# Performance work log

Hardware: AMD Instinct MI355X
Metric: run time of the kernel (lower is better)

Reference implementation:

```python
import jax, jax.numpy as jnp
import numpy as np

NC = 151  # number of object classes (VG)
NR = 51   # number of relation classes (VG)


def setup_inputs() -> dict:
    key = jax.random.key(0)
    ks = jax.random.split(key, 10)
    B, N, D = 32, 100, 4096
    H = D // 4
    w = lambda k, shape, fan_in: (jax.random.normal(k, shape, jnp.float32) / np.sqrt(fan_in).astype(np.float32))
    return {
        "encoder_reps": jax.random.normal(ks[0], (B * N, D), jnp.float32),
        "W_comp": w(ks[1], (D, H), D),        # obj_comp Linear (no bias)
        "W_ou1": w(ks[2], (H, H), H),         # ou1 Linear
        "W_ofc": w(ks[3], (H, H), H),         # ofc_u Linear
        "W_decomp": w(ks[4], (H, D), H),      # obj_decomp Linear
        "conv1": w(ks[5], (10, NR, 3, 3), NR * 9),  # Conv2d(51,10,3,pad=1)
        "conv2": w(ks[6], (5, 10, 3, 3), 10 * 9),   # Conv2d(10,5,3,pad=1)
        "conv3": w(ks[7], (1, 5, 1, 1), 5),         # Conv2d(5,1,1)
        "freq_emb": jax.random.normal(ks[8], (NC * NC, NR), jnp.float32) * 0.01,
        "obj_preds": jax.random.randint(ks[9], (B * N,), 0, NC),
        "num_obj": 100,
    }


def reference(encoder_reps, W_comp, W_ou1, W_ofc, W_decomp, conv1, conv2, conv3, freq_emb, obj_preds, num_obj):
    T, D = encoder_reps.shape
    N = num_obj
    B = T // N
    relu = jax.nn.relu
    # obj_comp then per-image ou1 (vectorized over images)
    comp = relu(encoder_reps @ W_comp).reshape(B, N, -1)   # [B,N,H]
    obj_u1 = relu(comp @ W_ou1)                             # [B,N,H]
    # product-index frequency-bias gather: emb[subj*NC + obj]
    labels = obj_preds.reshape(B, N)
    pair_idx = labels[:, :, None] * NC + labels[:, None, :]  # [B,N,N]
    adj_fg = freq_emb[pair_idx]                               # [B,N,N,NR]
    # adjacency net: Conv-Conv-Conv-Tanh over the NxN 'image' with NR channels
    x = jnp.transpose(adj_fg, (0, 3, 1, 2))                   # [B,NR,N,N]
    dn = ("NCHW", "OIHW", "NCHW")
    x = jax.lax.conv_general_dilated(x, conv1, (1, 1), "SAME", dimension_numbers=dn)
    x = jax.lax.conv_general_dilated(x, conv2, (1, 1), "SAME", dimension_numbers=dn)
    x = jnp.tanh(jax.lax.conv_general_dilated(x, conv3, (1, 1), "SAME", dimension_numbers=dn))
    adj = x[:, 0]                                             # [B,N,N]
    # graph message passing: adj @ obj_u1, then ofc_u / decomp + residual
    ofl_u = jnp.einsum("bnm,bmh->bnh", adj, obj_u1).reshape(T, -1)
    u_m = relu(ofl_u @ W_ofc)
    decomp = relu(u_m @ W_decomp)
    return decomp + encoder_reps
```

## Files before the change

### kernel.cpp

```cpp
#include <hip/hip_runtime.h>
#include <cmath>

#define NCC 151
#define NRCH 51
#define BDIM 32
#define NOBJ 100
#define DDIM 4096
#define HDIM 1024
#define TDIM (BDIM * NOBJ)

typedef __bf16 bf16_t;
typedef __bf16 bf16x8 __attribute__((ext_vector_type(8)));
typedef __bf16 bf16x4 __attribute__((ext_vector_type(4)));
typedef float f32x4 __attribute__((ext_vector_type(4)));

template <bool RELU, bool ADDBF16, int SPLITK, int MODE>
__global__ __launch_bounds__(256) void gemm_bf16(
    const bf16_t* __restrict__ A,
    const bf16_t* __restrict__ Bt,
    const bf16_t* __restrict__ add,
    void* __restrict__ Cout,
    int N, int K, size_t MN) {
  __shared__ __align__(16) bf16_t Asm[2][128 * 64];
  __shared__ __align__(16) bf16_t Bsm[2][128 * 64];
  const int tid = threadIdx.x;
  const int lane = tid & 63;
  const int w = tid >> 6;
  const int wm = w >> 1, wn = w & 1;

  const int nx = gridDim.x, ny = gridDim.y, nz = gridDim.z;
  const int h = blockIdx.x + nx * (blockIdx.y + ny * blockIdx.z);
  int bx, by, bz;
  if (MODE == 3) {
    const int xcd = h & 7, s = h >> 3;
    bz = xcd >> 1;
    const int half = xcd & 1;
    if (half == 1 && s >= 96) return;
    const int c = s / 40;
    if (c < 2) {
      const int within = s % 40;
      bx = within / 5;
      by = (half ? 13 : 0) + c * 5 + within % 5;
    } else if (half == 0) {
      const int w2 = s - 80;
      bx = w2 / 3;
      by = 10 + w2 % 3;
    } else {
      const int w2 = s - 80;
      bx = w2 / 2;
      by = 23 + w2 % 2;
    }
  } else {
    const int nwg = nx * ny * nz;
    const int q = nwg >> 3;
    const int lin = (h & 7) * q + (h >> 3);
    by = lin % ny;
    const int r = lin / ny;
    bx = r % nx;
    bz = r / nx;
  }

  const int bm = by * 128, bn = bx * 128;
  const int lr = lane & 15;
  const int lk = lane >> 4;

  int kBeg = 0, kEnd = K;
  if (SPLITK > 1) {
    const int chunk = (((K / 64) + SPLITK - 1) / SPLITK) * 64;
    kBeg = bz * chunk;
    kEnd = min(K, kBeg + chunk);
  }

  f32x4 acc[4][4];
#pragma unroll
  for (int m = 0; m < 4; ++m)
#pragma unroll
    for (int n = 0; n < 4; ++n) acc[m][n] = (f32x4){0.f, 0.f, 0.f, 0.f};

  const int srow = tid >> 3;
  const int sslot = tid & 7;

  auto stage = [&](int buf, int kt) {
#pragma unroll
    for (int i = 0; i < 4; ++i) {
      const int row = i * 32 + srow;
      const int kc = sslot ^ (row & 7);
      const bf16_t* ga = A + (size_t)(bm + row) * K + kt + kc * 8;
      const bf16_t* gb = Bt + (size_t)(bn + row) * K + kt + kc * 8;
      __builtin_amdgcn_global_load_lds(
          (const __attribute__((address_space(1))) void*)ga,
          (__attribute__((address_space(3))) void*)((char*)&Asm[buf][0] +
                                                    i * 4096 + w * 1024),
          16, 0, 0);
      __builtin_amdgcn_global_load_lds(
          (const __attribute__((address_space(1))) void*)gb,
          (__attribute__((address_space(3))) void*)((char*)&Bsm[buf][0] +
                                                    i * 4096 + w * 1024),
          16, 0, 0);
    }
  };

  stage(0, kBeg);
  __syncthreads();

  int cur = 0;
  for (int kt = kBeg; kt < kEnd; kt += 64) {
    const bool more = (kt + 64 < kEnd);
    if (more) stage(cur ^ 1, kt + 64);

    char* ldsA = (char*)&Asm[cur][0];
    char* ldsB = (char*)&Bsm[cur][0];
    bf16x8 af[4][2], bfr[4][2];
#pragma unroll
    for (int m = 0; m < 4; ++m) {
      const int row = wm * 64 + m * 16 + lr;
#pragma unroll
      for (int kk = 0; kk < 2; ++kk) {
        const int slot = kk * 4 + lk;
        af[m][kk] =
            *(const bf16x8*)(ldsA + row * 128 + ((slot ^ (lr & 7)) << 4));
      }
    }
#pragma unroll
    for (int n = 0; n < 4; ++n) {
      const int row = wn * 64 + n * 16 + lr;
#pragma unroll
      for (int kk = 0; kk < 2; ++kk) {
        const int slot = kk * 4 + lk;
        bfr[n][kk] =
            *(const bf16x8*)(ldsB + row * 128 + ((slot ^ (lr & 7)) << 4));
      }
    }
#pragma unroll
    for (int m = 0; m < 4; ++m)
#pragma unroll
      for (int n = 0; n < 4; ++n) {
        acc[m][n] = __builtin_amdgcn_mfma_f32_16x16x32_bf16(
            af[m][0], bfr[n][0], acc[m][n], 0, 0, 0);
        acc[m][n] = __builtin_amdgcn_mfma_f32_16x16x32_bf16(
            af[m][1], bfr[n][1], acc[m][n], 0, 0, 0);
      }

    if (more) __syncthreads();
    cur ^= 1;
  }

  const int or0 = bm + wm * 64 + lk * 4;
  const int oc0 = bn + wn * 64 + lr;
#pragma unroll
  for (int m = 0; m < 4; ++m)
#pragma unroll
    for (int n = 0; n < 4; ++n)
#pragma unroll
      for (int r = 0; r < 4; ++r) {
        float v = acc[m][n][r];
        const size_t off = (size_t)(or0 + m * 16 + r) * N + (oc0 + n * 16);
        if (SPLITK > 1) {
          ((bf16_t*)Cout)[bz * MN + off] = (bf16_t)v;
        } else {
          if (RELU) v = fmaxf(v, 0.f);
          if (ADDBF16)
            ((float*)Cout)[off] = v + (float)add[off];
          else
            ((bf16_t*)Cout)[off] = (bf16_t)v;
        }
      }
}

template <int NPART>
__global__ __launch_bounds__(256) void reduceN_kernel(
    const bf16_t* __restrict__ p, bf16_t* __restrict__ out, int n8,
    size_t MN) {
  int i = blockIdx.x * 256 + threadIdx.x;
  if (i >= n8) return;
  float s[8] = {};
#pragma unroll
  for (int z = 0; z < NPART; ++z) {
    bf16x8 v = *(const bf16x8*)(p + z * MN + (size_t)i * 8);
#pragma unroll
    for (int j = 0; j < 8; ++j) s[j] += (float)v[j];
  }
  bf16x8 o;
#pragma unroll
  for (int j = 0; j < 8; ++j) o[j] = (bf16_t)fmaxf(s[j], 0.f);
  *(bf16x8*)(out + (size_t)i * 8) = o;
}

__global__ __launch_bounds__(256) void cvt_bf16_kernel(
    const float* __restrict__ in, bf16_t* __restrict__ out, int n4) {
  int i = blockIdx.x * 256 + threadIdx.x;
  if (i >= n4) return;
  float4 v = ((const float4*)in)[i];
  bf16x4 o = {(bf16_t)v.x, (bf16_t)v.y, (bf16_t)v.z, (bf16_t)v.w};
  ((bf16x4*)out)[i] = o;
}

__global__ __launch_bounds__(256) void transT_kernel(
    const float* __restrict__ in, bf16_t* __restrict__ out, int K, int N) {
  __shared__ float t[32][33];
  const int n0 = blockIdx.x * 32, k0 = blockIdx.y * 32;
  const int tx = threadIdx.x & 31, ty = threadIdx.x >> 5;
#pragma unroll
  for (int i = 0; i < 4; ++i)
    t[ty + i * 8][tx] = in[(size_t)(k0 + ty + i * 8) * N + n0 + tx];
  __syncthreads();
#pragma unroll
  for (int i = 0; i < 4; ++i)
    out[(size_t)(n0 + ty + i * 8) * K + k0 + tx] = (bf16_t)t[tx][ty + i * 8];
}

__global__ __launch_bounds__(256) void prep_w1r_kernel(
    const float* __restrict__ w1, float* __restrict__ w1r) {
  int idx = blockIdx.x * 256 + threadIdx.x;
  if (idx >= NRCH * 90) return;
  int ci = idx / 90, r = idx % 90, k9 = r / 10, co = r % 10;
  w1r[idx] = w1[((co * NRCH + ci) * 3 + k9 / 3) * 3 + (k9 % 3)];
}

__global__ __launch_bounds__(128) void femb1_kernel(
    const float* __restrict__ femb, const float* __restrict__ w1r,
    float* __restrict__ femb1) {
  __shared__ float row[NRCH];
  const int p = blockIdx.x;
  if (threadIdx.x < NRCH)
    row[threadIdx.x] = femb[(size_t)p * NRCH + threadIdx.x];
  __syncthreads();
  const int t = threadIdx.x;
  if (t >= 90) return;
  float acc = 0.f;
#pragma unroll
  for (int ci = 0; ci < NRCH; ++ci) acc += row[ci] * w1r[ci * 90 + t];
  femb1[((size_t)p * 9 + t / 10) * 12 + (t % 10)] = acc;
}

__global__ __launch_bounds__(256) void conv1g_kernel(
    const int* __restrict__ preds, const float* __restrict__ femb1,
    float* __restrict__ x1) {
  int idx = blockIdx.x * 256 + threadIdx.x;
  if (idx >= BDIM * NOBJ * NOBJ) return;
  int j = idx % NOBJ;
  int i = (idx / NOBJ) % NOBJ;
  int b = idx / (NOBJ * NOBJ);
  const int* pr = preds + b * NOBJ;
  int li[3], lj[3];
#pragma unroll
  for (int d = 0; d < 3; ++d) {
    li[d] = pr[min(max(i + d - 1, 0), NOBJ - 1)];
    lj[d] = pr[min(max(j + d - 1, 0), NOBJ - 1)];
  }
  f32x4 a0 = {0.f, 0.f, 0.f, 0.f}, a1 = a0, a2 = a0;
#pragma unroll
  for (int kh = 0; kh < 3; ++kh) {
    int ii = i + kh - 1;
    if (ii < 0 || ii >= NOBJ) continue;
#pragma unroll
    for (int kw = 0; kw < 3; ++kw) {
      int jj = j + kw - 1;
      if (jj < 0 || jj >= NOBJ) continue;
      int p = li[kh] * NCC + lj[kw];
      const f32x4* f =
          (const f32x4*)(femb1 + ((size_t)p * 9 + kh * 3 + kw) * 12);
      a0 += f[0];
      a1 += f[1];
      a2 += f[2];
    }
  }
  f32x4* o = (f32x4*)(x1 + (size_t)idx * 12);
  o[0] = a0;
  o[1] = a1;
  o[2] = a2;
}

__global__ __launch_bounds__(256) void conv23_kernel(
    const float* __restrict__ x1, const float* __restrict__ w2,
    const float* __restrict__ w3, float* __restrict__ adj) {
  __shared__ float w[90];
  if (threadIdx.x < 90) {
    const int k9 = threadIdx.x / 10, c2 = threadIdx.x % 10;
    float a = 0.f;
#pragma unroll
    for (int c3 = 0; c3 < 5; ++c3)
      a += w3[c3] * w2[(c3 * 10 + c2) * 9 + k9];
    w[threadIdx.x] = a;
  }
  __syncthreads();
  int idx = blockIdx.x * 256 + threadIdx.x;
  if (idx >= BDIM * NOBJ * NOBJ) return;
  int j = idx % NOBJ;
  int i = (idx / NOBJ) % NOBJ;
  int b = idx / (NOBJ * NOBJ);
  float acc = 0.f;
  const float* xb = x1 + (size_t)b * NOBJ * NOBJ * 12;
#pragma unroll
  for (int kh = 0; kh < 3; ++kh) {
    int ii = i + kh - 1;
    if (ii < 0 || ii >= NOBJ) continue;
#pragma unroll
    for (int kw = 0; kw < 3; ++kw) {
      int jj = j + kw - 1;
      if (jj < 0 || jj >= NOBJ) continue;
      const float* xr = xb + (ii * NOBJ + jj) * 12;
      const float* wr = w + (kh * 3 + kw) * 10;
#pragma unroll
      for (int c = 0; c < 10; ++c) acc += wr[c] * xr[c];
    }
  }
  adj[idx] = tanhf(acc);
}

__global__ __launch_bounds__(256) void einsum_mfma_kernel(
    const float* __restrict__ adj,
    const bf16_t* __restrict__ u1,
    bf16_t* __restrict__ ofl) {
  __shared__ __align__(16) bf16_t As[128 * 128];
  __shared__ __align__(16) bf16_t Us[128 * 128];
  const int b = blockIdx.y;
  const int h0 = blockIdx.x * 128;
  const int tid = threadIdx.x, lane = tid & 63, w = tid >> 6;
  const int wm = w >> 1, wn = w & 1;
  const int lr = lane & 15, lk = lane >> 4;

  {
    f32x4 z = {0.f, 0.f, 0.f, 0.f};
#pragma unroll
    for (int i = 0; i < 8; ++i) ((f32x4*)As)[tid + i * 256] = z;
#pragma unroll
    for (int i = 0; i < 8; ++i) ((f32x4*)Us)[tid + i * 256] = z;
  }
  __syncthreads();

  const float* ab = adj + (size_t)b * 10000;
#pragma unroll
  for (int i = 0; i < 10; ++i) {
    int idx = tid + i * 256;
    if (idx < 2500) {
      int row = idx / 25, kc = idx % 25;
      f32x4 v = ((const f32x4*)ab)[idx];
      bf16x4 o = {(bf16_t)v[0], (bf16_t)v[1], (bf16_t)v[2], (bf16_t)v[3]};
      int slot = kc >> 1;
      *(bf16x4*)((char*)As + row * 256 + ((slot ^ (row & 7)) << 4) +
                 (kc & 1) * 8) = o;
    }
  }

  const bf16_t* ub = u1 + (size_t)b * 100 * HDIM + h0;
#pragma unroll
  for (int i = 0; i < 7; ++i) {
    int idx = tid + i * 256;
    if (idx < 1600) {
      int hc = idx / 100, m = idx % 100;
      bf16x8 v = *(const bf16x8*)(ub + (size_t)m * HDIM + hc * 8);
      int slot = m >> 3, mr = m & 7;
#pragma unroll
      for (int j = 0; j < 8; ++j) {
        int h = hc * 8 + j;
        *((bf16_t*)((char*)Us + h * 256 + ((slot ^ (h & 7)) << 4) + mr * 2)) =
            v[j];
      }
    }
  }
  __syncthreads();

  f32x4 acc[4][4];
#pragma unroll
  for (int m = 0; m < 4; ++m)
#pragma unroll
    for (int n = 0; n < 4; ++n) acc[m][n] = (f32x4){0.f, 0.f, 0.f, 0.f};

#pragma unroll
  for (int ks = 0; ks < 4; ++ks) {
    bf16x8 a[4], u[4];
#pragma unroll
    for (int m = 0; m < 4; ++m) {
      int row = wm * 64 + m * 16 + lr;
      int slot = ks * 4 + lk;
      a[m] = *(const bf16x8*)((char*)As + row * 256 + ((slot ^ (lr & 7)) << 4));
    }
#pragma unroll
    for (int n = 0; n < 4; ++n) {
      int row = wn * 64 + n * 16 + lr;
      int slot = ks * 4 + lk;
      u[n] = *(const bf16x8*)((char*)Us + row * 256 + ((slot ^ (lr & 7)) << 4));
    }
#pragma unroll
    for (int m = 0; m < 4; ++m)
#pragma unroll
      for (int n = 0; n < 4; ++n)
        acc[m][n] = __builtin_amdgcn_mfma_f32_16x16x32_bf16(a[m], u[n],
                                                            acc[m][n], 0, 0, 0);
  }

  const int or0 = wm * 64 + lk * 4;
  const int oc0 = h0 + wn * 64 + lr;
#pragma unroll
  for (int m = 0; m < 4; ++m)
#pragma unroll
    for (int n = 0; n < 4; ++n)
#pragma unroll
      for (int r = 0; r < 4; ++r) {
        int row = or0 + m * 16 + r;
        if (row < 100)
          ofl[((size_t)b * 100 + row) * HDIM + oc0 + n * 16] =
              (bf16_t)acc[m][n][r];
      }
}

extern "C" void kernel_launch(void* const* d_in, const int* in_sizes, int n_in,
                              void* d_out, int out_size, void* d_ws,
                              size_t ws_size, hipStream_t stream) {
  const float* enc = (const float*)d_in[0];
  const float* W_comp = (const float*)d_in[1];
  const float* W_ou1 = (const float*)d_in[2];
  const float* W_ofc = (const float*)d_in[3];
  const float* W_dec = (const float*)d_in[4];
  const float* conv1w = (const float*)d_in[5];
  const float* conv2w = (const float*)d_in[6];
  const float* conv3w = (const float*)d_in[7];
  const float* femb = (const float*)d_in[8];
  const int* preds = (const int*)d_in[9];
  float* out = (float*)d_out;
  char* wsb = (char*)d_ws;

  const size_t MN = (size_t)TDIM * HDIM;

  bf16_t* encb   = (bf16_t*)(wsb + 0);
  bf16_t* WcompT = (bf16_t*)(wsb + 26214400);
  bf16_t* comp   = (bf16_t*)(wsb + 34603008);
  bf16_t* part4  = (bf16_t*)(wsb + 41156608);
  bf16_t* Wou1T  = (bf16_t*)(wsb + 41156608);
  float*  femb1  = (float*)(wsb + 43272512);
  float*  w1r    = (float*)(wsb + 53122560);
  float*  x1     = (float*)(wsb + 54402560);
  bf16_t* obj_u1 = (bf16_t*)(wsb + 69762560);
  float*  adj    = (float*)(wsb + 76316160);
  bf16_t* ofl_u  = (bf16_t*)(wsb + 26214400);
  bf16_t* WofcT  = (bf16_t*)(wsb + 32768000);
  bf16_t* u_m    = (bf16_t*)(wsb + 34865152);
  bf16_t* WdecT  = (bf16_t*)(wsb + 41418752);

  const int n8 = (int)(MN / 8);

  cvt_bf16_kernel<<<(TDIM * DDIM / 4 + 255) / 256, 256, 0, stream>>>(
      enc, encb, TDIM * DDIM / 4);
  transT_kernel<<<dim3(HDIM / 32, DDIM / 32), 256, 0, stream>>>(
      W_comp, WcompT, DDIM, HDIM);

  gemm_bf16<false, false, 4, 3><<<dim3(832, 1, 1), 256, 0, stream>>>(
      encb, WcompT, nullptr, part4, HDIM, DDIM, MN);
  reduceN_kernel<4><<<n8 / 256, 256, 0, stream>>>(part4, comp, n8, MN);

  transT_kernel<<<dim3(HDIM / 32, HDIM / 32), 256, 0, stream>>>(
      W_ou1, Wou1T, HDIM, HDIM);
  gemm_bf16<true, false, 1, 0>
      <<<dim3(HDIM / 128, TDIM / 128), 256, 0, stream>>>(
          comp, Wou1T, nullptr, obj_u1, HDIM, HDIM, MN);

  prep_w1r_kernel<<<(NRCH * 90 + 255) / 256, 256, 0, stream>>>(conv1w, w1r);
  femb1_kernel<<<NCC * NCC, 128, 0, stream>>>(femb, w1r, femb1);
  conv1g_kernel<<<(BDIM * NOBJ * NOBJ + 255) / 256, 256, 0, stream>>>(
      preds, femb1, x1);
  conv23_kernel<<<(BDIM * NOBJ * NOBJ + 255) / 256, 256, 0, stream>>>(
      x1, conv2w, conv3w, adj);

  transT_kernel<<<dim3(HDIM / 32, HDIM / 32), 256, 0, stream>>>(
      W_ofc, WofcT, HDIM, HDIM);
  transT_kernel<<<dim3(DDIM / 32, HDIM / 32), 256, 0, stream>>>(
      W_dec, WdecT, HDIM, DDIM);

  einsum_mfma_kernel<<<dim3(HDIM / 128, BDIM), 256, 0, stream>>>(adj, obj_u1,
                                                                 ofl_u);

  gemm_bf16<true, false, 1, 0>
      <<<dim3(HDIM / 128, TDIM / 128), 256, 0, stream>>>(
          ofl_u, WofcT, nullptr, u_m, HDIM, HDIM, MN);

  gemm_bf16<true, true, 1, 0>
      <<<dim3(DDIM / 128, TDIM / 128), 256, 0, stream>>>(
          u_m, WdecT, encb, out, DDIM, HDIM, MN);
}
```

Baseline: 251.0 us.

## Use 256x256 GEMM tiles for big GEMMs and single-buffer the 128 kernel

Introduces a 512-thread 256x256-tile GEMM with row padding to 3328 and bounds-checked stores, used for the split-K obj_comp GEMM and the decomp GEMM. The hand-tuned XCD mapping is replaced by a generic remap. The 128-tile GEMM is simplified to single-buffered LDS with two barriers per k-step, and workspace offsets are shifted to make room for padded buffers. Larger tiles raise data reuse per block but reduce occupancy and drop the load/compute overlap from double buffering.

```diff
diff --git a/kernel.cpp b/kernel.cpp
--- a/kernel.cpp
+++ b/kernel.cpp
@@ -8,68 +8,34 @@
 #define DDIM 4096
 #define HDIM 1024
 #define TDIM (BDIM * NOBJ)
+#define MPAD 3328
 
 typedef __bf16 bf16_t;
 typedef __bf16 bf16x8 __attribute__((ext_vector_type(8)));
 typedef __bf16 bf16x4 __attribute__((ext_vector_type(4)));
 typedef float f32x4 __attribute__((ext_vector_type(4)));
 
-template <bool RELU, bool ADDBF16, int SPLITK, int MODE>
-__global__ __launch_bounds__(256) void gemm_bf16(
-    const bf16_t* __restrict__ A,
-    const bf16_t* __restrict__ Bt,
-    const bf16_t* __restrict__ add,
-    void* __restrict__ Cout,
-    int N, int K, size_t MN) {
-  __shared__ __align__(16) bf16_t Asm[2][128 * 64];
-  __shared__ __align__(16) bf16_t Bsm[2][128 * 64];
+template <bool RELU>
+__global__ __launch_bounds__(256) void gemm128(
+    const bf16_t* __restrict__ A, const bf16_t* __restrict__ Bt,
+    bf16_t* __restrict__ C, int N, int K) {
+  __shared__ __align__(16) bf16_t Asm[128 * 64];
+  __shared__ __align__(16) bf16_t Bsm[128 * 64];
   const int tid = threadIdx.x;
   const int lane = tid & 63;
   const int w = tid >> 6;
   const int wm = w >> 1, wn = w & 1;
 
-  const int nx = gridDim.x, ny = gridDim.y, nz = gridDim.z;
-  const int h = blockIdx.x + nx * (blockIdx.y + ny * blockIdx.z);
-  int bx, by, bz;
-  if (MODE == 3) {
-    const int xcd = h & 7, s = h >> 3;
-    bz = xcd >> 1;
-    const int half = xcd & 1;
-    if (half == 1 && s >= 96) return;
-    const int c = s / 40;
-    if (c < 2) {
-      const int within = s % 40;
-      bx = within / 5;
-      by = (half ? 13 : 0) + c * 5 + within % 5;
-    } else if (half == 0) {
-      const int w2 = s - 80;
-      bx = w2 / 3;
-      by = 10 + w2 % 3;
-    } else {
-      const int w2 = s - 80;
-      bx = w2 / 2;
-      by = 23 + w2 % 2;
-    }
-  } else {
-    const int nwg = nx * ny * nz;
-    const int q = nwg >> 3;
-    const int lin = (h & 7) * q + (h >> 3);
-    by = lin % ny;
-    const int r = lin / ny;
-    bx = r % nx;
-    bz = r / nx;
-  }
+  const int nx = gridDim.x, ny = gridDim.y;
+  const int h = blockIdx.x + nx * blockIdx.y;
+  const int nwg = nx * ny;
+  const int q = nwg >> 3;
+  const int lin = (h & 7) * q + (h >> 3);
+  const int by = lin % ny;
+  const int bx = lin / ny;
 
   const int bm = by * 128, bn = bx * 128;
-  const int lr = lane & 15;
-  const int lk = lane >> 4;
-
-  int kBeg = 0, kEnd = K;
-  if (SPLITK > 1) {
-    const int chunk = (((K / 64) + SPLITK - 1) / SPLITK) * 64;
-    kBeg = bz * chunk;
-    kEnd = min(K, kBeg + chunk);
-  }
+  const int lr = lane & 15, lk = lane >> 4;
 
   f32x4 acc[4][4];
 #pragma unroll
@@ -77,10 +43,12 @@
 #pragma unroll
     for (int n = 0; n < 4; ++n) acc[m][n] = (f32x4){0.f, 0.f, 0.f, 0.f};
 
-  const int srow = tid >> 3;
-  const int sslot = tid & 7;
-
-  auto stage = [&](int buf, int kt) {
+  const int srow = tid >> 3, sslot = tid & 7;
+  char* ldsA = (char*)Asm;
+  char* ldsB = (char*)Bsm;
+
+  for (int kt = 0; kt < K; kt += 64) {
+    __syncthreads();
 #pragma unroll
     for (int i = 0; i < 4; ++i) {
       const int row = i * 32 + srow;
@@ -89,27 +57,15 @@
       const bf16_t* gb = Bt + (size_t)(bn + row) * K + kt + kc * 8;
       __builtin_amdgcn_global_load_lds(
           (const __attribute__((address_space(1))) void*)ga,
-          (__attribute__((address_space(3))) void*)((char*)&Asm[buf][0] +
-                                                    i * 4096 + w * 1024),
+          (__attribute__((address_space(3))) void*)(ldsA + i * 4096 + w * 1024),
           16, 0, 0);
       __builtin_amdgcn_global_load_lds(
           (const __attribute__((address_space(1))) void*)gb,
-          (__attribute__((address_space(3))) void*)((char*)&Bsm[buf][0] +
-                                                    i * 4096 + w * 1024),
+          (__attribute__((address_space(3))) void*)(ldsB + i * 4096 + w * 1024),
           16, 0, 0);
     }
-  };
-
-  stage(0, kBeg);
-  __syncthreads();
-
-  int cur = 0;
-  for (int kt = kBeg; kt < kEnd; kt += 64) {
-    const bool more = (kt + 64 < kEnd);
-    if (more) stage(cur ^ 1, kt + 64);
-
-    char* ldsA = (char*)&Asm[cur][0];
-    char* ldsB = (char*)&Bsm[cur][0];
+    __syncthreads();
+
     bf16x8 af[4][2], bfr[4][2];
 #pragma unroll
     for (int m = 0; m < 4; ++m) {
@@ -140,9 +96,6 @@
         acc[m][n] = __builtin_amdgcn_mfma_f32_16x16x32_bf16(
             af[m][1], bfr[n][1], acc[m][n], 0, 0, 0);
       }
-
-    if (more) __syncthreads();
-    cur ^= 1;
   }
 
   const int or0 = bm + wm * 64 + lk * 4;
@@ -154,7 +107,110 @@
 #pragma unroll
       for (int r = 0; r < 4; ++r) {
         float v = acc[m][n][r];
-        const size_t off = (size_t)(or0 + m * 16 + r) * N + (oc0 + n * 16);
+        if (RELU) v = fmaxf(v, 0.f);
+        C[(size_t)(or0 + m * 16 + r) * N + (oc0 + n * 16)] = (bf16_t)v;
+      }
+}
+
+template <bool RELU, bool ADDBF16, int SPLITK>
+__global__ __launch_bounds__(512) void gemm256(
+    const bf16_t* __restrict__ A,
+    const bf16_t* __restrict__ Bt,
+    const bf16_t* __restrict__ add,
+    void* __restrict__ Cout,
+    int M, int N, int K, size_t MN) {
+  __shared__ __align__(16) bf16_t Asm[256 * 64];
+  __shared__ __align__(16) bf16_t Bsm[256 * 64];
+  const int tid = threadIdx.x;
+  const int lane = tid & 63;
+  const int w = tid >> 6;
+  const int wm = w >> 2, wn = w & 3;
+
+  const int nx = gridDim.x, ny = gridDim.y, nz = gridDim.z;
+  const int h = blockIdx.x + nx * (blockIdx.y + ny * blockIdx.z);
+  const int nwg = nx * ny * nz;
+  const int q = nwg >> 3;
+  const int lin = (h & 7) * q + (h >> 3);
+  const int by = lin % ny;
+  const int r2 = lin / ny;
+  const int bx = r2 % nx;
+  const int bz = r2 / nx;
+
+  const int bm = by * 256, bn = bx * 256;
+  const int lr = lane & 15, lk = lane >> 4;
+
+  int kBeg = 0, kEnd = K;
+  if (SPLITK > 1) {
+    const int chunk = K / SPLITK;
+    kBeg = bz * chunk;
+    kEnd = kBeg + chunk;
+  }
+
+  f32x4 acc[8][4];
+#pragma unroll
+  for (int m = 0; m < 8; ++m)
+#pragma unroll
+    for (int n = 0; n < 4; ++n) acc[m][n] = (f32x4){0.f, 0.f, 0.f, 0.f};
+
+  const int srow = tid >> 3;
+  const int sslot = tid & 7;
+  char* ldsA = (char*)Asm;
+  char* ldsB = (char*)Bsm;
+
+  for (int kt = kBeg; kt < kEnd; kt += 64) {
+    __syncthreads();
+#pragma unroll
+    for (int i = 0; i < 4; ++i) {
+      const int row = i * 64 + srow;
+      const int kc = sslot ^ (row & 7);
+      const bf16_t* ga = A + (size_t)(bm + row) * K + kt + kc * 8;
+      const bf16_t* gb = Bt + (size_t)(bn + row) * K + kt + kc * 8;
+      __builtin_amdgcn_global_load_lds(
+          (const __attribute__((address_space(1))) void*)ga,
+          (__attribute__((address_space(3))) void*)(ldsA + i * 8192 + w * 1024),
+          16, 0, 0);
+      __builtin_amdgcn_global_load_lds(
+          (const __attribute__((address_space(1))) void*)gb,
+          (__attribute__((address_space(3))) void*)(ldsB + i * 8192 + w * 1024),
+          16, 0, 0);
+    }
+    __syncthreads();
+
+#pragma unroll
+    for (int kk = 0; kk < 2; ++kk) {
+      bf16x8 af[8], bfr[4];
+      const int slot = kk * 4 + lk;
+#pragma unroll
+      for (int n = 0; n < 4; ++n) {
+        const int row = wn * 64 + n * 16 + lr;
+        bfr[n] = *(const bf16x8*)(ldsB + row * 128 + ((slot ^ (lr & 7)) << 4));
+      }
+#pragma unroll
+      for (int m = 0; m < 8; ++m) {
+        const int row = wm * 128 + m * 16 + lr;
+        af[m] = *(const bf16x8*)(ldsA + row * 128 + ((slot ^ (lr & 7)) << 4));
+      }
+#pragma unroll
+      for (int m = 0; m < 8; ++m)
+#pragma unroll
+        for (int n = 0; n < 4; ++n)
+          acc[m][n] = __builtin_amdgcn_mfma_f32_16x16x32_bf16(
+              af[m], bfr[n], acc[m][n], 0, 0, 0);
+    }
+  }
+
+  const int or0 = bm + wm * 128 + lk * 4;
+  const int oc0 = bn + wn * 64 + lr;
+#pragma unroll
+  for (int m = 0; m < 8; ++m)
+#pragma unroll
+    for (int n = 0; n < 4; ++n)
+#pragma unroll
+      for (int r = 0; r < 4; ++r) {
+        const int row = or0 + m * 16 + r;
+        if (row >= M) continue;
+        float v = acc[m][n][r];
+        const size_t off = (size_t)row * N + (oc0 + n * 16);
         if (SPLITK > 1) {
           ((bf16_t*)Cout)[bz * MN + off] = (bf16_t)v;
         } else {
@@ -309,8 +365,7 @@
 }
 
 __global__ __launch_bounds__(256) void einsum_mfma_kernel(
-    const float* __restrict__ adj,
-    const bf16_t* __restrict__ u1,
+    const float* __restrict__ adj, const bf16_t* __restrict__ u1,
     bf16_t* __restrict__ ofl) {
   __shared__ __align__(16) bf16_t As[128 * 128];
   __shared__ __align__(16) bf16_t Us[128 * 128];
@@ -424,19 +479,19 @@
   const size_t MN = (size_t)TDIM * HDIM;
 
   bf16_t* encb   = (bf16_t*)(wsb + 0);
-  bf16_t* WcompT = (bf16_t*)(wsb + 26214400);
-  bf16_t* comp   = (bf16_t*)(wsb + 34603008);
-  bf16_t* part4  = (bf16_t*)(wsb + 41156608);
-  bf16_t* Wou1T  = (bf16_t*)(wsb + 41156608);
-  float*  femb1  = (float*)(wsb + 43272512);
-  float*  w1r    = (float*)(wsb + 53122560);
-  float*  x1     = (float*)(wsb + 54402560);
-  bf16_t* obj_u1 = (bf16_t*)(wsb + 69762560);
-  float*  adj    = (float*)(wsb + 76316160);
-  bf16_t* ofl_u  = (bf16_t*)(wsb + 26214400);
-  bf16_t* WofcT  = (bf16_t*)(wsb + 32768000);
-  bf16_t* u_m    = (bf16_t*)(wsb + 34865152);
-  bf16_t* WdecT  = (bf16_t*)(wsb + 41418752);
+  bf16_t* WcompT = (bf16_t*)(wsb + 27262976);
+  bf16_t* comp   = (bf16_t*)(wsb + 35651584);
+  bf16_t* part4  = (bf16_t*)(wsb + 42205184);
+  bf16_t* Wou1T  = (bf16_t*)(wsb + 42205184);
+  float*  femb1  = (float*)(wsb + 44302336);
+  float*  w1r    = (float*)(wsb + 54152368);
+  float*  x1     = (float*)(wsb + 54170752);
+  bf16_t* obj_u1 = (bf16_t*)(wsb + 69530752);
+  float*  adj    = (float*)(wsb + 76084352);
+  bf16_t* ofl_u  = (bf16_t*)(wsb + 27262976);
+  bf16_t* WofcT  = (bf16_t*)(wsb + 33816576);
+  bf16_t* u_m    = (bf16_t*)(wsb + 35913728);
+  bf16_t* WdecT  = (bf16_t*)(wsb + 42729472);
 
   const int n8 = (int)(MN / 8);
 
@@ -445,15 +500,15 @@
   transT_kernel<<<dim3(HDIM / 32, DDIM / 32), 256, 0, stream>>>(
       W_comp, WcompT, DDIM, HDIM);
 
-  gemm_bf16<false, false, 4, 3><<<dim3(832, 1, 1), 256, 0, stream>>>(
-      encb, WcompT, nullptr, part4, HDIM, DDIM, MN);
+  gemm256<false, false, 4><<<dim3(HDIM / 256, MPAD / 256, 4), 512, 0,
+                             stream>>>(encb, WcompT, nullptr, part4, TDIM,
+                                       HDIM, DDIM, MN);
   reduceN_kernel<4><<<n8 / 256, 256, 0, stream>>>(part4, comp, n8, MN);
 
   transT_kernel<<<dim3(HDIM / 32, HDIM / 32), 256, 0, stream>>>(
       W_ou1, Wou1T, HDIM, HDIM);
-  gemm_bf16<true, false, 1, 0>
-      <<<dim3(HDIM / 128, TDIM / 128), 256, 0, stream>>>(
-          comp, Wou1T, nullptr, obj_u1, HDIM, HDIM, MN);
+  gemm128<true><<<dim3(HDIM / 128, TDIM / 128), 256, 0, stream>>>(
+      comp, Wou1T, obj_u1, HDIM, HDIM);
 
   prep_w1r_kernel<<<(NRCH * 90 + 255) / 256, 256, 0, stream>>>(conv1w, w1r);
   femb1_kernel<<<NCC * NCC, 128, 0, stream>>>(femb, w1r, femb1);
@@ -470,11 +525,9 @@
   einsum_mfma_kernel<<<dim3(HDIM / 128, BDIM), 256, 0, stream>>>(adj, obj_u1,
                                                                  ofl_u);
 
-  gemm_bf16<true, false, 1, 0>
-      <<<dim3(HDIM / 128, TDIM / 128), 256, 0, stream>>>(
-          ofl_u, WofcT, nullptr, u_m, HDIM, HDIM, MN);
-
-  gemm_bf16<true, true, 1, 0>
-      <<<dim3(DDIM / 128, TDIM / 128), 256, 0, stream>>>(
-          u_m, WdecT, encb, out, DDIM, HDIM, MN);
-}
+  gemm128<true><<<dim3(HDIM / 128, TDIM / 128), 256, 0, stream>>>(
+      ofl_u, WofcT, u_m, HDIM, HDIM);
+
+  gemm256<true, true, 1><<<dim3(DDIM / 256, MPAD / 256, 1), 512, 0, stream>>>(
+      u_m, WdecT, encb, out, TDIM, DDIM, HDIM, MN);
+}
```

New measurement: 251.8 us. About the same (+0.3%).
